# Performance work log

Measured on AMD Instinct MI355X. Metric: run time of the kernel, lower is better.

The kernel has to match this reference:

```python
import jax, jax.numpy as jnp
import numpy as np

N_NODES = 100000
N_EDGES = 200000
N_GRAPHS = 128
F_NODE, F_EDGE, F_GRAPH = 32, 16, 8
D, D_LIN, D_OUT = 32, 128, 1
MP_TIMES, STEPS = 3, 3


def setup_inputs() -> dict:
    key = jax.random.key(0)
    ks = jax.random.split(key, 26)
    p = lambda i, shape: jax.random.normal(ks[i], shape, dtype=jnp.float32) * 0.1
    return {
        "x": jax.random.normal(ks[0], (N_NODES, F_NODE), dtype=jnp.float32),
        "edge_attr": jax.random.normal(ks[1], (N_EDGES, F_EDGE), dtype=jnp.float32),
        "graph_attr": jax.random.normal(ks[2], (N_GRAPHS, F_GRAPH), dtype=jnp.float32),
        "edge_index": jax.random.randint(ks[3], (2, N_EDGES), 0, N_NODES),
        "batch": jnp.sort(jax.random.randint(ks[4], (N_NODES,), 0, N_GRAPHS)),
        "lin0_w": p(5, (F_NODE, D)), "lin0_b": p(6, (D,)),
        "nn1_w": p(7, (F_EDGE, D_LIN)), "nn1_b": p(8, (D_LIN,)),
        "nn2_w": p(9, (D_LIN, D * D)), "nn2_b": p(10, (D * D,)),
        "root_w": p(11, (D, D)), "conv_b": p(12, (D,)),
        "gru_wih": p(13, (D, 3 * D)), "gru_whh": p(14, (D, 3 * D)),
        "gru_bih": p(15, (3 * D,)), "gru_bhh": p(16, (3 * D,)),
        "lstm_wih": p(17, (2 * D, 4 * D)), "lstm_whh": p(18, (D, 4 * D)),
        "lstm_bih": p(19, (4 * D,)), "lstm_bhh": p(20, (4 * D,)),
        "lin1_w": p(21, (2 * D + F_GRAPH, D)), "lin1_b": p(22, (D,)),
        "lin2_w": p(23, (D, D_OUT)), "lin2_b": p(24, (D_OUT,)),
    }


def reference(x, edge_attr, graph_attr, edge_index, batch,
              lin0_w, lin0_b, nn1_w, nn1_b, nn2_w, nn2_b, root_w, conv_b,
              gru_wih, gru_whh, gru_bih, gru_bhh,
              lstm_wih, lstm_whh, lstm_bih, lstm_bhh,
              lin1_w, lin1_b, lin2_w, lin2_b):
    N = x.shape[0]
    G = graph_attr.shape[0]
    Dd = lin0_w.shape[1]
    src, dst = edge_index[0], edge_index[1]

    out = jax.nn.relu(x @ lin0_w + lin0_b)        # [N, D]
    h = out                                        # GRU hidden state

    # edge-conditioned weight matrices: MLP(edge_attr) -> [E, D, D]
    ew = (jax.nn.relu(edge_attr @ nn1_w + nn1_b) @ nn2_w + nn2_b).reshape(-1, Dd, Dd)
    deg = jnp.maximum(
        jax.ops.segment_sum(jnp.ones(src.shape[0], out.dtype), dst, num_segments=N), 1.0)

    for _ in range(MP_TIMES):
        # NNConv (aggr='mean'): gather-matmul-scatter + root transform
        msg = jnp.einsum('ed,edo->eo', out[src], ew)                 # [E, D]
        agg = jax.ops.segment_sum(msg, dst, num_segments=N) / deg[:, None]
        m = jax.nn.relu(out @ root_w + agg + conv_b)
        # GRU cell (torch gate order r, z, n)
        gi = m @ gru_wih + gru_bih
        gh = h @ gru_whh + gru_bhh
        i_r, i_z, i_n = jnp.split(gi, 3, axis=-1)
        h_r, h_z, h_n = jnp.split(gh, 3, axis=-1)
        r = jax.nn.sigmoid(i_r + h_r)
        z = jax.nn.sigmoid(i_z + h_z)
        n = jnp.tanh(i_n + r * h_n)
        h = (1.0 - z) * n + z * h
        out = h

    # Set2Set attention pooling (LSTM gate order i, f, g, o)
    q_star = jnp.zeros((G, 2 * Dd), out.dtype)
    hs = jnp.zeros((G, Dd), out.dtype)
    cs = jnp.zeros((G, Dd), out.dtype)
    for _ in range(STEPS):
        g = q_star @ lstm_wih + lstm_bih + hs @ lstm_whh + lstm_bhh
        ig, fg, gg, og = jnp.split(g, 4, axis=-1)
        cs = jax.nn.sigmoid(fg) * cs + jax.nn.sigmoid(ig) * jnp.tanh(gg)
        hs = jax.nn.sigmoid(og) * jnp.tanh(cs)                        # query [G, D]
        e = jnp.sum(out * hs[batch], axis=-1)                         # [N]
        emax = jax.ops.segment_max(e, batch, num_segments=G)
        w = jnp.exp(e - emax[batch])
        denom = jax.ops.segment_sum(w, batch, num_segments=G)
        a = w / denom[batch]                                          # segment softmax
        rvec = jax.ops.segment_sum(a[:, None] * out, batch, num_segments=G)
        q_star = jnp.concatenate([hs, rvec], axis=-1)

    z = jax.nn.relu(jnp.concatenate([q_star, graph_attr], axis=1) @ lin1_w + lin1_b)
    return z @ lin2_w + lin2_b
```

## Files before the change

kernel.cpp:

```cpp
#include <hip/hip_runtime.h>
#include <stdint.h>
#include <stddef.h>

#define NND 100000
#define NED 200000
#define NG  128

typedef unsigned short us4v __attribute__((ext_vector_type(4)));
typedef short bf16x8 __attribute__((ext_vector_type(8)));
typedef float f32x4 __attribute__((ext_vector_type(4)));

__device__ __forceinline__ float bf2f(unsigned short u){
  union{unsigned u; float f;} v; v.u = ((unsigned)u)<<16; return v.f;
}
__device__ __forceinline__ unsigned short f2bf(float f){
  union{float f; unsigned u;} v; v.f = f;
  unsigned r = v.u + 0x7FFFu + ((v.u>>16)&1u);
  return (unsigned short)(r>>16);
}
__device__ __forceinline__ float sigm(float x){ return 1.f/(1.f+__expf(-x)); }
__device__ __forceinline__ float tanh_(float x){ return 2.f/(1.f+__expf(-2.f*x)) - 1.f; }

static const size_t kNeed = 90000000ull;
static void* g_fb = nullptr;
namespace {
struct FB { FB(){ if (hipMalloc(&g_fb, kNeed) != hipSuccess) g_fb = nullptr; } };
static FB g_fb_init;
}


__global__ __launch_bounds__(256) void k_misc(const float* __restrict__ nn2, const float* __restrict__ b2,
                                              unsigned short* __restrict__ Btbl, float* __restrict__ b2tl,
                                              const int* __restrict__ batch,
                                              int* __restrict__ starts, int* __restrict__ counts,
                                              float* __restrict__ deg, float* __restrict__ agg){
  int b = blockIdx.x;
  if (b < 512){
    int t = b*256 + threadIdx.x;
    int j  = t & 7;
    int ln = (t >> 3) & 63;
    int ni = (t >> 9) & 3;
    int ks = (t >> 11) & 3;
    int wc = (t >> 13) & 1;
    int cg = t >> 14;
    int k = ks*32 + (ln >> 4)*8 + j;
    int o = wc*16 + (ln & 15);
    int d = cg*4 + ni;
    Btbl[t] = f2bf(nn2[(k << 10) + d*32 + o]);
    if (t < 1024){
      int ni2 = t & 3, r2 = (t >> 2) & 15, wc2 = (t >> 6) & 1, cg2 = t >> 7;
      int o2 = wc2*16 + r2, d2 = cg2*4 + ni2;
      b2tl[t] = b2[d2*32 + o2];
    }
  } else if (b == 512){
    __shared__ int s[129];
    int g = threadIdx.x;
    if (g < 128){
      int lo = 0, hi = NND;
      while (lo < hi){ int mid = (lo + hi) >> 1; if (batch[mid] < g) lo = mid + 1; else hi = mid; }
      s[g] = lo;
      if (g == 0) s[128] = NND;
    }
    __syncthreads();
    if (g < 128){ starts[g] = s[g]; counts[g] = s[g+1] - s[g]; }
  } else {
    int idx = (b - 513)*256 + threadIdx.x;
    const int stride = 511*256;
    float4 z; z.x=0.f; z.y=0.f; z.z=0.f; z.w=0.f;
    for (int i = idx; i < (NND*32)/4; i += stride) ((float4*)agg)[i] = z;
    for (int i = idx; i < NND; i += stride) deg[i] = 0.f;
  }
}

__global__ __launch_bounds__(256) void k_lin0(const float* __restrict__ x, const float* __restrict__ w,
                                              const float* __restrict__ b, float* __restrict__ cur){
  __shared__ float sw[1024]; __shared__ float sb[32];
  __shared__ float sx[8][32];
  for (int i = threadIdx.x; i < 1024; i += 256) sw[i] = w[i];
  if (threadIdx.x < 32) sb[threadIdx.x] = b[threadIdx.x];
  __syncthreads();
  int ln = threadIdx.x >> 5, j = threadIdx.x & 31;
  for (int it = 0; it < 4; ++it){
    int n = (blockIdx.x*4 + it)*8 + ln;
    if (n >= NND) return;
    float xj = x[(size_t)n*32 + j];
    sx[ln][j] = xj;
    float acc = sb[j];
    #pragma unroll
    for (int d=0; d<32; d++) acc += sx[ln][d]*sw[d*32+j];
    cur[(size_t)n*32 + j] = fmaxf(acc, 0.f);
  }
}

__global__ __launch_bounds__(256) void k_hidden(const float* __restrict__ ea, const float* __restrict__ w1,
                                                const float* __restrict__ b1, unsigned short* __restrict__ H){
  __shared__ float sw[2048]; __shared__ float sb[128];
  for (int i=threadIdx.x;i<2048;i+=256) sw[i]=w1[i];
  if (threadIdx.x<128) sb[threadIdx.x]=b1[threadIdx.x];
  __syncthreads();
  int gid = blockIdx.x*256 + threadIdx.x;
  int e = gid >> 5, q = gid & 31;
  float a[16];
  const float4* ap = (const float4*)(ea + (size_t)e*16);
  #pragma unroll
  for (int i=0;i<4;i++){ float4 v=ap[i]; a[4*i]=v.x; a[4*i+1]=v.y; a[4*i+2]=v.z; a[4*i+3]=v.w; }
  float c0=sb[q*4], c1=sb[q*4+1], c2=sb[q*4+2], c3=sb[q*4+3];
  #pragma unroll
  for (int k=0;k<16;k++){
    float av=a[k]; const float* wr = &sw[k*128 + q*4];
    c0 += av*wr[0]; c1 += av*wr[1]; c2 += av*wr[2]; c3 += av*wr[3];
  }
  us4v o;
  o[0]=f2bf(fmaxf(c0,0.f)); o[1]=f2bf(fmaxf(c1,0.f));
  o[2]=f2bf(fmaxf(c2,0.f)); o[3]=f2bf(fmaxf(c3,0.f));
  *(us4v*)(H + (size_t)e*128 + q*4) = o;
}

__global__ __launch_bounds__(256) void k_deg(const int* __restrict__ dst, float* __restrict__ deg){
  int e = blockIdx.x*256 + threadIdx.x;
  if (e < NED) atomicAdd(&deg[dst[e]], 1.f);
}

__global__ __launch_bounds__(256) void k_msgf(const unsigned short* __restrict__ Hb,
                                              const unsigned short* __restrict__ Btbl,
                                              const float* __restrict__ b2tl,
                                              const float* __restrict__ cur,
                                              const int* __restrict__ src, const int* __restrict__ dst,
                                              float* __restrict__ agg){
  __shared__ char smem[32768];
  char* sA = smem;
  float* s_o  = (float*)smem;
  int*   s_dst = (int*)(smem + 18432);
  int tid = threadIdx.x;
  int e0 = blockIdx.x * 128;
  int l = tid & 63, wv = tid >> 6;
  int wr = wv >> 1, wc = wv & 1;
  int r = l & 15, hi = l >> 4;
  const bf16x8* Bfrag = (const bf16x8*)Btbl;
  const float4* b2t4 = (const float4*)b2tl;

  {
    int rr = tid >> 4, c16 = (tid & 15) * 16;
    #pragma unroll
    for (int pass = 0; pass < 8; ++pass){
      int row = pass*16 + rr;
      int ge = e0 + row; if (ge >= NED) ge = NED - 1;
      bf16x8 v = *(const bf16x8*)(Hb + (size_t)ge*128 + (tid&15)*8);
      *(bf16x8*)(sA + row*256 + (c16 ^ ((row&7)<<4))) = v;
    }
  }
  __syncthreads();
  bf16x8 afr[4][4];
  #pragma unroll
  for (int mi=0; mi<4; ++mi){
    int row = wr*64 + mi*16 + r;
    #pragma unroll
    for (int ks=0; ks<4; ++ks){
      int kb = ks*64 + hi*16;
      afr[mi][ks] = *(bf16x8*)(sA + row*256 + (kb ^ ((row&7)<<4)));
    }
  }
  __syncthreads();

  if (tid < 128) s_dst[tid] = dst[min(e0 + tid, NED-1)];
  #pragma unroll
  for (int pass=0; pass<4; ++pass){
    int idx = pass*256 + tid;
    int row = idx >> 3, c4 = (idx & 7)*4;
    int sE = src[min(e0 + row, NED-1)];
    float4 v = *(const float4*)(cur + (size_t)sE*32 + c4);
    *(float4*)(s_o + row*36 + c4) = v;
  }
  __syncthreads();

  float macc[4][4] = {};

  for (int cg = 0; cg < 8; ++cg){
    float4 bzv = b2t4[(cg*2 + wc)*16 + r];
    f32x4 acc[4][4];
    #pragma unroll
    for (int mi=0; mi<4; ++mi)
      #pragma unroll
      for (int ni=0; ni<4; ++ni){
        float bb = (ni==0)?bzv.x:(ni==1)?bzv.y:(ni==2)?bzv.z:bzv.w;
        f32x4 a; a[0]=bb; a[1]=bb; a[2]=bb; a[3]=bb;
        acc[mi][ni] = a;
      }
    #pragma unroll
    for (int ks=0; ks<4; ++ks){
      bf16x8 bfr[4];
      #pragma unroll
      for (int ni=0; ni<4; ++ni)
        bfr[ni] = Bfrag[(size_t)((((cg*2 + wc)*4 + ks)*4 + ni)*64) + l];
      #pragma unroll
      for (int mi=0; mi<4; ++mi)
        #pragma unroll
        for (int ni=0; ni<4; ++ni)
          acc[mi][ni] = __builtin_amdgcn_mfma_f32_16x16x32_bf16(afr[mi][ks], bfr[ni], acc[mi][ni], 0, 0, 0);
    }
    #pragma unroll
    for (int mi=0; mi<4; ++mi)
      #pragma unroll
      for (int q=0; q<4; ++q){
        int e = wr*64 + mi*16 + hi*4 + q;
        float4 od = *(const float4*)(s_o + e*36 + cg*4);
        macc[mi][q] += acc[mi][0][q]*od.x + acc[mi][1][q]*od.y
                     + acc[mi][2][q]*od.z + acc[mi][3][q]*od.w;
      }
  }
  #pragma unroll
  for (int mi=0; mi<4; ++mi)
    #pragma unroll
    for (int q=0; q<4; ++q){
      int e = wr*64 + mi*16 + hi*4 + q;
      if (e0 + e < NED)
        atomicAdd(&agg[(size_t)s_dst[e]*32 + wc*16 + r], macc[mi][q]);
    }
}

__global__ __launch_bounds__(256) void k_gru(float* __restrict__ cur, float* __restrict__ agg,
                                             const float* __restrict__ deg,
                                             const float* __restrict__ root_w, const float* __restrict__ conv_b,
                                             const float* __restrict__ wih, const float* __restrict__ whh,
                                             const float* __restrict__ bih, const float* __restrict__ bhh){
  __shared__ float s_root[1024], s_wih[3072], s_whh[3072], s_cb[32], s_bih[96], s_bhh[96];
  __shared__ float s_c[32][32], s_m[32][32];
  for (int i=threadIdx.x;i<1024;i+=256) s_root[i]=root_w[i];
  for (int i=threadIdx.x;i<3072;i+=256){ s_wih[i]=wih[i]; s_whh[i]=whh[i]; }
  if (threadIdx.x<32) s_cb[threadIdx.x]=conv_b[threadIdx.x];
  if (threadIdx.x<96){ s_bih[threadIdx.x]=bih[threadIdx.x]; s_bhh[threadIdx.x]=bhh[threadIdx.x]; }
  __syncthreads();
  int ln = threadIdx.x >> 5, j = threadIdx.x & 31;
  int base = blockIdx.x * 160;
  for (int g4 = 0; g4 < 5; ++g4){
    float c[4], a[4], idg[4];
    int n[4];
    #pragma unroll
    for (int t=0;t<4;++t){
      n[t] = base + (g4*4 + t)*8 + ln;
      c[t] = cur[(size_t)n[t]*32 + j];
      a[t] = agg[(size_t)n[t]*32 + j];
      agg[(size_t)n[t]*32 + j] = 0.f;
      idg[t] = 1.f / fmaxf(deg[n[t]], 1.f);
      s_c[t*8+ln][j] = c[t];
    }
    float mm[4] = {};
    #pragma unroll 8
    for (int d=0; d<32; ++d){
      float w = s_root[d*32+j];
      #pragma unroll
      for (int t=0;t<4;++t) mm[t] += s_c[t*8+ln][d] * w;
    }
    float m[4];
    #pragma unroll
    for (int t=0;t<4;++t){
      m[t] = fmaxf(mm[t] + a[t]*idg[t] + s_cb[j], 0.f);
      s_m[t*8+ln][j] = m[t];
    }
    float gr[4], gz[4], gn[4], hr[4], hz[4], hh[4];
    #pragma unroll
    for (int t=0;t<4;++t){
      gr[t]=s_bih[j]; gz[t]=s_bih[32+j]; gn[t]=s_bih[64+j];
      hr[t]=s_bhh[j]; hz[t]=s_bhh[32+j]; hh[t]=s_bhh[64+j];
    }
    #pragma unroll 4
    for (int k=0;k<32;++k){
      float w0=s_wih[k*96+j], w1=s_wih[k*96+32+j], w2=s_wih[k*96+64+j];
      float v0=s_whh[k*96+j], v1=s_whh[k*96+32+j], v2=s_whh[k*96+64+j];
      #pragma unroll
      for (int t=0;t<4;++t){
        float mk=s_m[t*8+ln][k], ck=s_c[t*8+ln][k];
        gr[t]+=mk*w0; gz[t]+=mk*w1; gn[t]+=mk*w2;
        hr[t]+=ck*v0; hz[t]+=ck*v1; hh[t]+=ck*v2;
      }
    }
    #pragma unroll
    for (int t=0;t<4;++t){
      float r = sigm(gr[t]+hr[t]);
      float z = sigm(gz[t]+hz[t]);
      float nnv = tanh_(gn[t] + r*hh[t]);
      cur[(size_t)n[t]*32 + j] = (1.f-z)*nnv + z*c[t];
    }
  }
}

__global__ __launch_bounds__(256) void k_s2s(const float* __restrict__ cur,
                                             const int* __restrict__ starts, const int* __restrict__ counts,
                                             const float* __restrict__ ga,
                                             const float* __restrict__ lwih, const float* __restrict__ lwhh,
                                             const float* __restrict__ lbih, const float* __restrict__ lbhh,
                                             const float* __restrict__ w1, const float* __restrict__ b1,
                                             const float* __restrict__ w2, const float* __restrict__ b2,
                                             float* __restrict__ ev, float* __restrict__ out){
  int g = blockIdx.x;
  int s0 = starts[g], cnt = counts[g];
  int tid = threadIdx.x;
  __shared__ float hs[32], cs[32], rv[32], sg[128];
  __shared__ float red[256];
  if (tid < 32){ hs[tid]=0.f; cs[tid]=0.f; rv[tid]=0.f; }
  __syncthreads();
  for (int step=0; step<3; ++step){
    if (tid < 128){
      int j = tid;
      float acc = lbih[j] + lbhh[j];
      #pragma unroll 8
      for (int k=0;k<32;k++){
        acc += hs[k]*(lwih[k*128+j] + lwhh[k*128+j]);
        acc += rv[k]*lwih[(32+k)*128+j];
      }
      sg[j] = acc;
    }
    __syncthreads();
    if (tid < 32){
      int j = tid;
      float cn = sigm(sg[32+j])*cs[j] + sigm(sg[j])*tanh_(sg[64+j]);
      cs[j] = cn;
      hs[j] = sigm(sg[96+j])*tanh_(cn);
    }
    __syncthreads();
    float lmax = -3.4e38f;
    for (int i = tid; i < cnt; i += 256){
      const float4* cp = (const float4*)(cur + (size_t)(s0+i)*32);
      float acc = 0.f;
      #pragma unroll
      for (int q=0;q<8;q++){ float4 v=cp[q]; acc += v.x*hs[q*4]+v.y*hs[q*4+1]+v.z*hs[q*4+2]+v.w*hs[q*4+3]; }
      ev[s0+i] = acc;
      lmax = fmaxf(lmax, acc);
    }
    red[tid] = lmax; __syncthreads();
    #pragma unroll
    for (int st=128; st>0; st>>=1){ if (tid<st) red[tid]=fmaxf(red[tid],red[tid+st]); __syncthreads(); }
    float mx = red[0]; __syncthreads();
    float vec[32];
    #pragma unroll
    for (int k=0;k<32;k++) vec[k]=0.f;
    float lsum = 0.f;
    for (int i = tid; i < cnt; i += 256){
      float w = __expf(ev[s0+i]-mx);
      lsum += w;
      const float4* cp = (const float4*)(cur + (size_t)(s0+i)*32);
      #pragma unroll
      for (int q=0;q<8;q++){ float4 v=cp[q]; vec[q*4]+=w*v.x; vec[q*4+1]+=w*v.y; vec[q*4+2]+=w*v.z; vec[q*4+3]+=w*v.w; }
    }
    red[tid] = lsum; __syncthreads();
    #pragma unroll
    for (int st=128; st>0; st>>=1){ if (tid<st) red[tid]+=red[tid+st]; __syncthreads(); }
    float inv = 1.f/red[0];
    if (tid < 32) rv[tid] = 0.f;
    __syncthreads();
    #pragma unroll
    for (int k=0;k<32;k++){
      float v = vec[k];
      #pragma unroll
      for (int o=32;o>0;o>>=1) v += __shfl_down(v, o, 64);
      if ((tid&63)==0) atomicAdd(&rv[k], v);
    }
    __syncthreads();
    if (tid < 32) rv[tid] *= inv;
    __syncthreads();
  }
  if (tid < 32){
    int j = tid;
    float acc = b1[j];
    #pragma unroll 8
    for (int k=0;k<32;k++) acc += hs[k]*w1[k*32+j];
    #pragma unroll 8
    for (int k=0;k<32;k++) acc += rv[k]*w1[(32+k)*32+j];
    #pragma unroll
    for (int k=0;k<8;k++)  acc += ga[g*8+k]*w1[(64+k)*32+j];
    float r = fmaxf(acc, 0.f)*w2[j];
    #pragma unroll
    for (int o=16;o>0;o>>=1) r += __shfl_down(r, o, 64);
    if (j == 0) out[g] = r + b2[0];
  }
}

extern "C" void kernel_launch(void* const* d_in, const int* in_sizes, int n_in,
                              void* d_out, int out_size, void* d_ws, size_t ws_size,
                              hipStream_t stream){
  (void)in_sizes; (void)n_in; (void)out_size;
  const float* x         = (const float*)d_in[0];
  const float* edge_attr = (const float*)d_in[1];
  const float* graph_attr= (const float*)d_in[2];
  const int*   eidx      = (const int*)d_in[3];
  const int*   batch     = (const int*)d_in[4];
  const float* lin0_w    = (const float*)d_in[5];
  const float* lin0_b    = (const float*)d_in[6];
  const float* nn1_w     = (const float*)d_in[7];
  const float* nn1_b     = (const float*)d_in[8];
  const float* nn2_w     = (const float*)d_in[9];
  const float* nn2_b     = (const float*)d_in[10];
  const float* root_w    = (const float*)d_in[11];
  const float* conv_b    = (const float*)d_in[12];
  const float* gru_wih   = (const float*)d_in[13];
  const float* gru_whh   = (const float*)d_in[14];
  const float* gru_bih   = (const float*)d_in[15];
  const float* gru_bhh   = (const float*)d_in[16];
  const float* lstm_wih  = (const float*)d_in[17];
  const float* lstm_whh  = (const float*)d_in[18];
  const float* lstm_bih  = (const float*)d_in[19];
  const float* lstm_bhh  = (const float*)d_in[20];
  const float* lin1_w    = (const float*)d_in[21];
  const float* lin1_b    = (const float*)d_in[22];
  const float* lin2_w    = (const float*)d_in[23];
  const float* lin2_b    = (const float*)d_in[24];
  const int* src = eidx;
  const int* dst = eidx + NED;

  char* pool = (ws_size >= kNeed) ? (char*)d_ws : (char*)g_fb;
  if (!pool) pool = (char*)d_ws;
  size_t off = 0;
  auto alloc = [&](size_t bytes)->char* {
    char* p = pool + off; off += (bytes + 511) & ~(size_t)511; return p;
  };
  unsigned short* H   = (unsigned short*)alloc((size_t)NED*128*2);
  float* cur  = (float*)alloc((size_t)NND*32*4);
  float* agg  = (float*)alloc((size_t)NND*32*4);
  float* deg  = (float*)alloc((size_t)NND*4);
  float* ev   = (float*)alloc((size_t)NND*4);
  unsigned short* Btbl = (unsigned short*)alloc(1024*128*2);
  float* b2tl = (float*)alloc(1024*4);
  int*   counts = (int*)alloc(512);
  int*   startsb= (int*)alloc(512);

  k_misc<<<1024, 256, 0, stream>>>(nn2_w, nn2_b, Btbl, b2tl, batch, startsb, counts, deg, agg);
  k_lin0<<<(NND+31)/32, 256, 0, stream>>>(x, lin0_w, lin0_b, cur);
  k_hidden<<<NED*32/256, 256, 0, stream>>>(edge_attr, nn1_w, nn1_b, H);
  k_deg<<<(NED+255)/256, 256, 0, stream>>>(dst, deg);

  for (int it=0; it<3; ++it){
    k_msgf<<<(NED+127)/128, 256, 0, stream>>>(H, Btbl, b2tl, cur, src, dst, agg);
    k_gru<<<625, 256, 0, stream>>>(cur, agg, deg, root_w, conv_b,
                                   gru_wih, gru_whh, gru_bih, gru_bhh);
  }
  k_s2s<<<NG, 256, 0, stream>>>(cur, startsb, counts, graph_attr,
                                lstm_wih, lstm_whh, lstm_bih, lstm_bhh,
                                lin1_w, lin1_b, lin2_w, lin2_b, ev, (float*)d_out);
}
```

Before: 515.1 us.

## Fuse lin0 and edge-hidden kernels into setup kernel; shrink message tile to 96 edges

The lin0 projection and the edge-MLP hidden-layer kernels are merged into the existing setup kernel as additional block ranges, which removes two launches and lets these independent jobs share one grid. The message-passing kernel tile drops from 128 to 96 edges per block, so each wave handles 3 row tiles instead of 4. This means more blocks, less shared memory and fewer registers per block, in exchange for reloading the B fragments more often. The fused kernel now statically reserves shared memory for every branch, which may reduce its occupancy.

```diff
diff --git a/kernel.cpp b/kernel.cpp
--- a/kernel.cpp
+++ b/kernel.cpp
@@ -5,6 +5,11 @@
 #define NND 100000
 #define NED 200000
 #define NG  128
+
+#define EB 96
+#define MSGF_GRID ((NED + EB - 1) / EB)
+#define HID_BLOCKS (NED*32/256)
+#define LIN0_BLOCKS ((NND + 31) / 32)
 
 typedef unsigned short us4v __attribute__((ext_vector_type(4)));
 typedef short bf16x8 __attribute__((ext_vector_type(8)));
@@ -33,7 +38,15 @@
                                               unsigned short* __restrict__ Btbl, float* __restrict__ b2tl,
                                               const int* __restrict__ batch,
                                               int* __restrict__ starts, int* __restrict__ counts,
-                                              float* __restrict__ deg, float* __restrict__ agg){
+                                              float* __restrict__ deg, float* __restrict__ agg,
+                                              const float* __restrict__ ea, const float* __restrict__ w1,
+                                              const float* __restrict__ b1, unsigned short* __restrict__ H,
+                                              const float* __restrict__ x, const float* __restrict__ w0,
+                                              const float* __restrict__ b0, float* __restrict__ cur){
+  __shared__ float swh[2048]; __shared__ float sbh[128];
+  __shared__ float sw0[1024]; __shared__ float sb0[32];
+  __shared__ float sx0[8][32];
+  __shared__ int s[129];
   int b = blockIdx.x;
   if (b < 512){
     int t = b*256 + threadIdx.x;
@@ -53,7 +66,6 @@
       b2tl[t] = b2[d2*32 + o2];
     }
   } else if (b == 512){
-    __shared__ int s[129];
     int g = threadIdx.x;
     if (g < 128){
       int lo = 0, hi = NND;
@@ -63,57 +75,49 @@
     }
     __syncthreads();
     if (g < 128){ starts[g] = s[g]; counts[g] = s[g+1] - s[g]; }
-  } else {
+  } else if (b < 1024){
     int idx = (b - 513)*256 + threadIdx.x;
     const int stride = 511*256;
     float4 z; z.x=0.f; z.y=0.f; z.z=0.f; z.w=0.f;
     for (int i = idx; i < (NND*32)/4; i += stride) ((float4*)agg)[i] = z;
     for (int i = idx; i < NND; i += stride) deg[i] = 0.f;
-  }
-}
-
-__global__ __launch_bounds__(256) void k_lin0(const float* __restrict__ x, const float* __restrict__ w,
-                                              const float* __restrict__ b, float* __restrict__ cur){
-  __shared__ float sw[1024]; __shared__ float sb[32];
-  __shared__ float sx[8][32];
-  for (int i = threadIdx.x; i < 1024; i += 256) sw[i] = w[i];
-  if (threadIdx.x < 32) sb[threadIdx.x] = b[threadIdx.x];
-  __syncthreads();
-  int ln = threadIdx.x >> 5, j = threadIdx.x & 31;
-  for (int it = 0; it < 4; ++it){
-    int n = (blockIdx.x*4 + it)*8 + ln;
-    if (n >= NND) return;
-    float xj = x[(size_t)n*32 + j];
-    sx[ln][j] = xj;
-    float acc = sb[j];
-    #pragma unroll
-    for (int d=0; d<32; d++) acc += sx[ln][d]*sw[d*32+j];
-    cur[(size_t)n*32 + j] = fmaxf(acc, 0.f);
-  }
-}
-
-__global__ __launch_bounds__(256) void k_hidden(const float* __restrict__ ea, const float* __restrict__ w1,
-                                                const float* __restrict__ b1, unsigned short* __restrict__ H){
-  __shared__ float sw[2048]; __shared__ float sb[128];
-  for (int i=threadIdx.x;i<2048;i+=256) sw[i]=w1[i];
-  if (threadIdx.x<128) sb[threadIdx.x]=b1[threadIdx.x];
-  __syncthreads();
-  int gid = blockIdx.x*256 + threadIdx.x;
-  int e = gid >> 5, q = gid & 31;
-  float a[16];
-  const float4* ap = (const float4*)(ea + (size_t)e*16);
-  #pragma unroll
-  for (int i=0;i<4;i++){ float4 v=ap[i]; a[4*i]=v.x; a[4*i+1]=v.y; a[4*i+2]=v.z; a[4*i+3]=v.w; }
-  float c0=sb[q*4], c1=sb[q*4+1], c2=sb[q*4+2], c3=sb[q*4+3];
-  #pragma unroll
-  for (int k=0;k<16;k++){
-    float av=a[k]; const float* wr = &sw[k*128 + q*4];
-    c0 += av*wr[0]; c1 += av*wr[1]; c2 += av*wr[2]; c3 += av*wr[3];
-  }
-  us4v o;
-  o[0]=f2bf(fmaxf(c0,0.f)); o[1]=f2bf(fmaxf(c1,0.f));
-  o[2]=f2bf(fmaxf(c2,0.f)); o[3]=f2bf(fmaxf(c3,0.f));
-  *(us4v*)(H + (size_t)e*128 + q*4) = o;
+  } else if (b < 1024 + HID_BLOCKS){
+    for (int i=threadIdx.x;i<2048;i+=256) swh[i]=w1[i];
+    if (threadIdx.x<128) sbh[threadIdx.x]=b1[threadIdx.x];
+    __syncthreads();
+    int gid = (b - 1024)*256 + threadIdx.x;
+    int e = gid >> 5, q = gid & 31;
+    float a[16];
+    const float4* ap = (const float4*)(ea + (size_t)e*16);
+    #pragma unroll
+    for (int i=0;i<4;i++){ float4 v=ap[i]; a[4*i]=v.x; a[4*i+1]=v.y; a[4*i+2]=v.z; a[4*i+3]=v.w; }
+    float c0=sbh[q*4], c1=sbh[q*4+1], c2=sbh[q*4+2], c3=sbh[q*4+3];
+    #pragma unroll
+    for (int k=0;k<16;k++){
+      float av=a[k]; const float* wr = &swh[k*128 + q*4];
+      c0 += av*wr[0]; c1 += av*wr[1]; c2 += av*wr[2]; c3 += av*wr[3];
+    }
+    us4v o;
+    o[0]=f2bf(fmaxf(c0,0.f)); o[1]=f2bf(fmaxf(c1,0.f));
+    o[2]=f2bf(fmaxf(c2,0.f)); o[3]=f2bf(fmaxf(c3,0.f));
+    *(us4v*)(H + (size_t)e*128 + q*4) = o;
+  } else {
+    for (int i = threadIdx.x; i < 1024; i += 256) sw0[i] = w0[i];
+    if (threadIdx.x < 32) sb0[threadIdx.x] = b0[threadIdx.x];
+    __syncthreads();
+    int lb = b - (1024 + HID_BLOCKS);
+    int ln = threadIdx.x >> 5, j = threadIdx.x & 31;
+    for (int it = 0; it < 4; ++it){
+      int n = (lb*4 + it)*8 + ln;
+      if (n >= NND) return;
+      float xj = x[(size_t)n*32 + j];
+      sx0[ln][j] = xj;
+      float acc = sb0[j];
+      #pragma unroll
+      for (int d=0; d<32; d++) acc += sx0[ln][d]*sw0[d*32+j];
+      cur[(size_t)n*32 + j] = fmaxf(acc, 0.f);
+    }
+  }
 }
 
 __global__ __launch_bounds__(256) void k_deg(const int* __restrict__ dst, float* __restrict__ deg){
@@ -127,12 +131,12 @@
                                               const float* __restrict__ cur,
                                               const int* __restrict__ src, const int* __restrict__ dst,
                                               float* __restrict__ agg){
-  __shared__ char smem[32768];
+  __shared__ char smem[EB*256];
   char* sA = smem;
   float* s_o  = (float*)smem;
-  int*   s_dst = (int*)(smem + 18432);
+  int*   s_dst = (int*)(smem + 13824);
   int tid = threadIdx.x;
-  int e0 = blockIdx.x * 128;
+  int e0 = blockIdx.x * EB;
   int l = tid & 63, wv = tid >> 6;
   int wr = wv >> 1, wc = wv & 1;
   int r = l & 15, hi = l >> 4;
@@ -142,7 +146,7 @@
   {
     int rr = tid >> 4, c16 = (tid & 15) * 16;
     #pragma unroll
-    for (int pass = 0; pass < 8; ++pass){
+    for (int pass = 0; pass < 6; ++pass){
       int row = pass*16 + rr;
       int ge = e0 + row; if (ge >= NED) ge = NED - 1;
       bf16x8 v = *(const bf16x8*)(Hb + (size_t)ge*128 + (tid&15)*8);
@@ -150,10 +154,10 @@
     }
   }
   __syncthreads();
-  bf16x8 afr[4][4];
+  bf16x8 afr[3][4];
   #pragma unroll
-  for (int mi=0; mi<4; ++mi){
-    int row = wr*64 + mi*16 + r;
+  for (int mi=0; mi<3; ++mi){
+    int row = wr*48 + mi*16 + r;
     #pragma unroll
     for (int ks=0; ks<4; ++ks){
       int kb = ks*64 + hi*16;
@@ -162,9 +166,9 @@
   }
   __syncthreads();
 
-  if (tid < 128) s_dst[tid] = dst[min(e0 + tid, NED-1)];
+  if (tid < EB) s_dst[tid] = dst[min(e0 + tid, NED-1)];
   #pragma unroll
-  for (int pass=0; pass<4; ++pass){
+  for (int pass=0; pass<3; ++pass){
     int idx = pass*256 + tid;
     int row = idx >> 3, c4 = (idx & 7)*4;
     int sE = src[min(e0 + row, NED-1)];
@@ -173,13 +177,13 @@
   }
   __syncthreads();
 
-  float macc[4][4] = {};
+  float macc[3][4] = {};
 
   for (int cg = 0; cg < 8; ++cg){
     float4 bzv = b2t4[(cg*2 + wc)*16 + r];
-    f32x4 acc[4][4];
-    #pragma unroll
-    for (int mi=0; mi<4; ++mi)
+    f32x4 acc[3][4];
+    #pragma unroll
+    for (int mi=0; mi<3; ++mi)
       #pragma unroll
       for (int ni=0; ni<4; ++ni){
         float bb = (ni==0)?bzv.x:(ni==1)?bzv.y:(ni==2)?bzv.z:bzv.w;
@@ -193,26 +197,26 @@
       for (int ni=0; ni<4; ++ni)
         bfr[ni] = Bfrag[(size_t)((((cg*2 + wc)*4 + ks)*4 + ni)*64) + l];
       #pragma unroll
-      for (int mi=0; mi<4; ++mi)
+      for (int mi=0; mi<3; ++mi)
         #pragma unroll
         for (int ni=0; ni<4; ++ni)
           acc[mi][ni] = __builtin_amdgcn_mfma_f32_16x16x32_bf16(afr[mi][ks], bfr[ni], acc[mi][ni], 0, 0, 0);
     }
     #pragma unroll
-    for (int mi=0; mi<4; ++mi)
+    for (int mi=0; mi<3; ++mi)
       #pragma unroll
       for (int q=0; q<4; ++q){
-        int e = wr*64 + mi*16 + hi*4 + q;
+        int e = wr*48 + mi*16 + hi*4 + q;
         float4 od = *(const float4*)(s_o + e*36 + cg*4);
         macc[mi][q] += acc[mi][0][q]*od.x + acc[mi][1][q]*od.y
                      + acc[mi][2][q]*od.z + acc[mi][3][q]*od.w;
       }
   }
   #pragma unroll
-  for (int mi=0; mi<4; ++mi)
+  for (int mi=0; mi<3; ++mi)
     #pragma unroll
     for (int q=0; q<4; ++q){
-      int e = wr*64 + mi*16 + hi*4 + q;
+      int e = wr*48 + mi*16 + hi*4 + q;
       if (e0 + e < NED)
         atomicAdd(&agg[(size_t)s_dst[e]*32 + wc*16 + r], macc[mi][q]);
     }
@@ -423,13 +427,13 @@
   int*   counts = (int*)alloc(512);
   int*   startsb= (int*)alloc(512);
 
-  k_misc<<<1024, 256, 0, stream>>>(nn2_w, nn2_b, Btbl, b2tl, batch, startsb, counts, deg, agg);
-  k_lin0<<<(NND+31)/32, 256, 0, stream>>>(x, lin0_w, lin0_b, cur);
-  k_hidden<<<NED*32/256, 256, 0, stream>>>(edge_attr, nn1_w, nn1_b, H);
+  k_misc<<<1024 + HID_BLOCKS + LIN0_BLOCKS, 256, 0, stream>>>(
+      nn2_w, nn2_b, Btbl, b2tl, batch, startsb, counts, deg, agg,
+      edge_attr, nn1_w, nn1_b, H, x, lin0_w, lin0_b, cur);
   k_deg<<<(NED+255)/256, 256, 0, stream>>>(dst, deg);
 
   for (int it=0; it<3; ++it){
-    k_msgf<<<(NED+127)/128, 256, 0, stream>>>(H, Btbl, b2tl, cur, src, dst, agg);
+    k_msgf<<<MSGF_GRID, 256, 0, stream>>>(H, Btbl, b2tl, cur, src, dst, agg);
     k_gru<<<625, 256, 0, stream>>>(cur, agg, deg, root_w, conv_b,
                                    gru_wih, gru_whh, gru_bih, gru_bhh);
   }
```

Measured after the change: 473.2 us. 8.1% less time.
